# Kernel optimization log

Measured on AMD Instinct MI355X. Metric: run time of the kernel, lower is better.

Reference implementation:

```python
import jax, jax.numpy as jnp
import numpy as np

N_NODES = 50000
N_EDGES = 1000000
IN_CH = 128
OUT_CH = 128
N_HEADS = 8
CIS = 8.0


def _edge_conv(x, e, wq, bq, wk, bk, wv, bv, n_heads, cis):
    """One EdgeConv layer (PyG mean aggregation, source_to_target flow)."""
    src, dst = e[0], e[1]                       # x_j = x[src], x_i = x[dst]
    xi = x[dst]
    xj = x[src]
    feat = jnp.concatenate([xi, xj - xi], axis=1)        # [E, 2C]
    q = feat @ wq + bq                                   # [E, O]
    k = feat @ wk + bk
    v = feat @ wv + bv
    E, O = q.shape
    hs = O // n_heads
    q = q.reshape(E, n_heads, hs)
    k = k.reshape(E, n_heads, hs)
    v = v.reshape(E, n_heads, hs)
    # edge_weight = sign(log|dst-src| - log(cis))
    d = jnp.abs(dst - src).astype(q.dtype)
    ew = jnp.sign(jnp.log(d) - jnp.log(jnp.asarray(cis, q.dtype)))
    v = v * ew[:, None, None]
    scale = jnp.asarray(1.0 / np.sqrt(hs), q.dtype)
    probs = jax.nn.softmax(q * k * scale, axis=-1)       # softmax over head_size
    ctx = (probs * v).reshape(E, O)                      # [E, O]
    n = x.shape[0]
    s = jax.ops.segment_sum(ctx, dst, num_segments=n)    # mean aggr over targets
    cnt = jax.ops.segment_sum(jnp.ones((E,), ctx.dtype), dst, num_segments=n)
    return s / jnp.maximum(cnt, 1.0)[:, None]


def setup_inputs() -> dict:
    key = jax.random.key(0)
    ks = jax.random.split(key, 24)
    x = jax.random.normal(ks[0], (N_NODES, IN_CH), jnp.float32)
    edge_index = jax.random.randint(ks[1], (2, N_EDGES), 0, N_NODES, dtype=jnp.int32)
    half = N_EDGES // 2
    e0 = edge_index[:, jax.random.permutation(ks[2], N_EDGES)[:half]]
    e1 = edge_index[:, jax.random.permutation(ks[3], N_EDGES)[:half]]
    e2 = edge_index[:, jax.random.permutation(ks[4], N_EDGES)[:half]]
    batch = jnp.zeros((N_NODES,), jnp.int32)

    def mk(k, i, o):
        return jax.random.normal(k, (i, o), jnp.float32) * 0.02

    def mkb(k, o):
        return jax.random.normal(k, (o,), jnp.float32) * 0.02

    # layer dims: conv0 128->128, conv1 128->64, conv2 64->128
    return dict(
        x=x, e0=e0, e1=e1, e2=e2, batch=batch,
        wq0=mk(ks[5], 2 * IN_CH, OUT_CH), bq0=mkb(ks[6], OUT_CH),
        wk0=mk(ks[7], 2 * IN_CH, OUT_CH), bk0=mkb(ks[8], OUT_CH),
        wv0=mk(ks[9], 2 * IN_CH, OUT_CH), bv0=mkb(ks[10], OUT_CH),
        wq1=mk(ks[11], 2 * OUT_CH, OUT_CH // 2), bq1=mkb(ks[12], OUT_CH // 2),
        wk1=mk(ks[13], 2 * OUT_CH, OUT_CH // 2), bk1=mkb(ks[14], OUT_CH // 2),
        wv1=mk(ks[15], 2 * OUT_CH, OUT_CH // 2), bv1=mkb(ks[16], OUT_CH // 2),
        wq2=mk(ks[17], OUT_CH, OUT_CH), bq2=mkb(ks[18], OUT_CH),
        wk2=mk(ks[19], OUT_CH, OUT_CH), bk2=mkb(ks[20], OUT_CH),
        wv2=mk(ks[21], OUT_CH, OUT_CH), bv2=mkb(ks[22], OUT_CH),
    )


def reference(x, e0, e1, e2, batch,
              wq0, bq0, wk0, bk0, wv0, bv0,
              wq1, bq1, wk1, bk1, wv1, bv1,
              wq2, bq2, wk2, bk2, wv2, bv2):
    x0 = jax.nn.relu(_edge_conv(x, e0, wq0, bq0, wk0, bk0, wv0, bv0, N_HEADS, CIS))
    h = jax.nn.relu(_edge_conv(x0, e1, wq1, bq1, wk1, bk1, wv1, bv1, N_HEADS, CIS))
    h = _edge_conv(h, e2, wq2, bq2, wk2, bk2, wv2, bv2, N_HEADS, CIS)
    return jax.nn.relu(h + x0)
```

## Files before the change

kernel.cpp:

```cpp
#include <hip/hip_runtime.h>
#include <hip/hip_fp16.h>


typedef _Float16 f16x8 __attribute__((ext_vector_type(8)));
typedef unsigned int u32x4 __attribute__((ext_vector_type(4)));
typedef float f32x4 __attribute__((ext_vector_type(4)));
typedef float f32x2 __attribute__((ext_vector_type(2)));

__device__ __forceinline__ unsigned short f2h(float f) {
  __half h = __float2half(f);
  return *reinterpret_cast<unsigned short*>(&h);
}
__device__ __forceinline__ __half2 ash2(unsigned w) {
  return *reinterpret_cast<__half2*>(&w);
}

__device__ __forceinline__ void pack_w_seg(const float* __restrict__ wq,
                                           const float* __restrict__ wk,
                                           const float* __restrict__ wv,
                                           unsigned short* __restrict__ dst,
                                           int IN, int O, float kscale, int id) {
  int kchunks = IN >> 5, nchunks = O >> 4;
  int total = 6 * nchunks * kchunks * 64;
  if (id >= total) return;
  int lane = id & 63;
  int frag = id >> 6;
  int kc = frag % kchunks;
  int nc = (frag / kchunks) % nchunks;
  int mat = frag / (kchunks * nchunks);
  const float* w = (mat % 3 == 0) ? wq : (mat % 3 == 1) ? wk : wv;
  float mul = (mat % 3 == 1) ? kscale : 1.0f;
  int n = nc * 16 + (lane & 15);
  int k0 = kc * 32 + (lane >> 4) * 8;
  unsigned short tmp[8];
#pragma unroll
  for (int j = 0; j < 8; ++j) {
    int row = k0 + j;
    float bot = w[(size_t)(IN + row) * O + n];
    float val = (mat < 3) ? (w[(size_t)row * O + n] - bot) : bot;
    tmp[j] = f2h(val * mul);
  }
  uint4 o;
  o.x = (unsigned)tmp[0] | ((unsigned)tmp[1] << 16);
  o.y = (unsigned)tmp[2] | ((unsigned)tmp[3] << 16);
  o.z = (unsigned)tmp[4] | ((unsigned)tmp[5] << 16);
  o.w = (unsigned)tmp[6] | ((unsigned)tmp[7] << 16);
  reinterpret_cast<uint4*>(dst)[id] = o;
}

__device__ __forceinline__ void pack_b_seg(const float* __restrict__ bq,
                                           const float* __restrict__ bk,
                                           const float* __restrict__ bv, float kscale, int O,
                                           float* __restrict__ out, int i) {
  int mat = i / O, c = i % O;
  float v = 0.f;
  if (mat == 0) v = bq[c];
  else if (mat == 1) v = bk[c] * kscale;
  else if (mat == 2) v = bv[c];
  out[i] = v;
}

__global__ void preproc(
    const int* __restrict__ e0, const int* __restrict__ e1, const int* __restrict__ e2,
    int E, int* __restrict__ hist, int* __restrict__ rank, int NP,
    uint4* __restrict__ za, int na, uint4* __restrict__ zb, int nb,
    const float* __restrict__ x, unsigned short* __restrict__ xb, int n8,
    const float* __restrict__ wq0, const float* __restrict__ wk0, const float* __restrict__ wv0,
    const float* __restrict__ wq1, const float* __restrict__ wk1, const float* __restrict__ wv1,
    const float* __restrict__ wq2, const float* __restrict__ wk2, const float* __restrict__ wv2,
    unsigned short* __restrict__ wp0, unsigned short* __restrict__ wp1,
    unsigned short* __restrict__ wp2,
    const float* __restrict__ bq0, const float* __restrict__ bk0, const float* __restrict__ bv0,
    const float* __restrict__ bq1, const float* __restrict__ bk1, const float* __restrict__ bv1,
    const float* __restrict__ bq2, const float* __restrict__ bk2, const float* __restrict__ bv2,
    float* __restrict__ bias0, float* __restrict__ bias1, float* __restrict__ bias2,
    float sc16, float sc8) {
  const int tid = blockIdx.x * blockDim.x + threadIdx.x;
  const int stride = gridDim.x * blockDim.x;

  for (int i = tid; i < E; i += stride) {
    rank[i] = atomicAdd(&hist[e0[E + i]], 1);
    rank[(size_t)E + i] = atomicAdd(&hist[NP + e1[E + i]], 1);
    rank[2 * (size_t)E + i] = atomicAdd(&hist[2 * NP + e2[E + i]], 1);
  }

  const uint4 Z = make_uint4(0u, 0u, 0u, 0u);
  for (int j = tid; j < na; j += stride) za[j] = Z;
  for (int j = tid; j < nb; j += stride) zb[j] = Z;
  for (int j = tid; j < n8; j += stride) {
    float4 a = reinterpret_cast<const float4*>(x)[2 * j];
    float4 b = reinterpret_cast<const float4*>(x)[2 * j + 1];
    uint4 o;
    o.x = (unsigned)f2h(a.x) | ((unsigned)f2h(a.y) << 16);
    o.y = (unsigned)f2h(a.z) | ((unsigned)f2h(a.w) << 16);
    o.z = (unsigned)f2h(b.x) | ((unsigned)f2h(b.y) << 16);
    o.w = (unsigned)f2h(b.z) | ((unsigned)f2h(b.w) << 16);
    reinterpret_cast<uint4*>(xb)[j] = o;
  }
  if (tid < 12288) pack_w_seg(wq0, wk0, wv0, wp0, 128, 128, sc16, tid);
  else if (tid < 18432) pack_w_seg(wq1, wk1, wv1, wp1, 128, 64, sc8, tid - 12288);
  else if (tid < 24576) pack_w_seg(wq2, wk2, wv2, wp2, 64, 128, sc16, tid - 18432);
  else if (tid < 24576 + 1920) {
    int i = tid - 24576;
    if (i < 768) pack_b_seg(bq0, bk0, bv0, sc16, 128, bias0, i);
    else if (i < 1152) pack_b_seg(bq1, bk1, bv1, sc8, 64, bias1, i - 768);
    else pack_b_seg(bq2, bk2, bv2, sc16, 128, bias2, i - 1152);
  }
}

__device__ __forceinline__ int block_scan_excl256(int v, int* buf, int t, int* total) {
  buf[t] = v;
  __syncthreads();
#pragma unroll
  for (int off = 1; off < 256; off <<= 1) {
    int add = (t >= off) ? buf[t - off] : 0;
    __syncthreads();
    buf[t] += add;
    __syncthreads();
  }
  int incl = buf[t];
  *total = buf[255];
  __syncthreads();
  return incl - v;
}

__global__ void scan_pass1(const int* __restrict__ hist, int* __restrict__ excl,
                           int* __restrict__ bsum, int n, int NP) {
  __shared__ int buf[256];
  int y = blockIdx.y, t = threadIdx.x;
  int i = blockIdx.x * 256 + t;
  int v = (i < n) ? hist[y * NP + i] : 0;
  int total;
  int ex = block_scan_excl256(v, buf, t, &total);
  if (i < NP) excl[y * NP + i] = ex;
  if (t == 0) bsum[y * 256 + blockIdx.x] = total;
}

__global__ void scan_pass2(int* __restrict__ bsum, int nblk) {
  __shared__ int buf[256];
  int y = blockIdx.y, t = threadIdx.x;
  int v = (t < nblk) ? bsum[y * 256 + t] : 0;
  int total;
  int ex = block_scan_excl256(v, buf, t, &total);
  bsum[y * 256 + t] = ex;
}

__global__ void scan_pass3(const int* __restrict__ excl, const int* __restrict__ bsum,
                           int* __restrict__ rowptr, int n, int NP, int RP, int E) {
  int y = blockIdx.y;
  int i = blockIdx.x * 256 + threadIdx.x;
  if (i < n) rowptr[y * RP + i] = excl[y * NP + i] + bsum[y * 256 + blockIdx.x];
  if (i == 0) rowptr[y * RP + n] = E;
}

__global__ void scatter3(const int* __restrict__ e0, const int* __restrict__ e1,
                         const int* __restrict__ e2, int E, const int* __restrict__ rowptr,
                         const int* __restrict__ rank, long long* __restrict__ pairs,
                         int NP, int RP) {
  int y = blockIdx.y;
  const int* e = (y == 0) ? e0 : (y == 1) ? e1 : e2;
  int i = blockIdx.x * 256 + threadIdx.x;
  if (i >= E) return;
  int sN = e[i], d = e[E + i];
  int pos = rowptr[y * RP + d] + rank[(size_t)y * E + i];
  long long val = ((long long)(unsigned)d << 32) | (unsigned)sN;
  __builtin_nontemporal_store(val, &pairs[(size_t)y * E + pos]);
}

template <int IN, int O, int G>
__global__ __launch_bounds__(256, 4) void node_gemm(
    const unsigned short* __restrict__ xb, int N, int NT,
    const unsigned short* __restrict__ wpack, const float* __restrict__ bias6,
    unsigned short* __restrict__ Y1, unsigned short* __restrict__ Y2) {
  constexpr int KC = IN / 32;
  constexpr int NCH = O / 16;
  constexpr int CHR = IN / 8;
  constexpr int CM = CHR - 1;
  __shared__ unsigned short tiles[64 * IN];

  const int chunk = gridDim.x >> 3;
  const int lb = (blockIdx.x & 7) * chunk + (blockIdx.x >> 3);
  if (lb >= NT * G) return;
  const int tile = lb / G;
  const int grp = lb % G;

  const int t = threadIdx.x, w = t >> 6, ln = t & 63;
  const int n0 = tile * 64;

  {
    constexpr int RPI = 64 / CHR;
    constexpr int NI = 16 / RPI;
    const int r_in = ln / CHR, c = ln % CHR;
#pragma unroll
    for (int i = 0; i < NI; ++i) {
      int row = w * 16 + i * RPI + r_in;
      int node = min(n0 + row, N - 1);
      int sc = c ^ (row & CM);
      const unsigned short* g = xb + (size_t)node * IN + sc * 8;
      unsigned short* l = &tiles[(size_t)(w * 16 + i * RPI) * IN];
      __builtin_amdgcn_global_load_lds(
          (const __attribute__((address_space(1))) unsigned int*)g,
          (__attribute__((address_space(3))) unsigned int*)l, 16, 0, 0);
    }
  }
  __syncthreads();

  const int col = ln & 15, quad = ln >> 4;
  const int g0 = grp * 8 + w * 2;

  f32x4 acc[2][4];
#pragma unroll
  for (int cc = 0; cc < 2; ++cc)
#pragma unroll
    for (int m = 0; m < 4; ++m) acc[cc][m] = (f32x4){0.f, 0.f, 0.f, 0.f};

#pragma unroll
  for (int kc = 0; kc < KC; ++kc) {
    f16x8 a[4];
#pragma unroll
    for (int m = 0; m < 4; ++m) {
      int row = m * 16 + col;
      int sc = (kc * 4 + quad) ^ (row & CM);
      a[m] = *reinterpret_cast<const f16x8*>(&tiles[(size_t)row * IN + sc * 8]);
    }
#pragma unroll
    for (int cc = 0; cc < 2; ++cc) {
      const f16x8 b = *reinterpret_cast<const f16x8*>(
          wpack + ((size_t)((g0 + cc) * KC + kc) * 64 + ln) * 8);
#pragma unroll
      for (int m = 0; m < 4; ++m)
        acc[cc][m] = __builtin_amdgcn_mfma_f32_16x16x32_f16(a[m], b, acc[cc][m], 0, 0, 0);
    }
  }

#pragma unroll
  for (int cc = 0; cc < 2; ++cc) {
    int gch = g0 + cc;
    int mat = gch / NCH, ncg = gch % NCH;
    unsigned short* Yp = (mat < 3) ? Y1 : Y2;
    int mo = (mat < 3) ? mat : mat - 3;
    float bv = bias6[gch * 16 + col];
    size_t coloff = (size_t)mo * O + ncg * 16 + col;
#pragma unroll
    for (int m = 0; m < 4; ++m)
#pragma unroll
      for (int r = 0; r < 4; ++r) {
        int node = n0 + m * 16 + quad * 4 + r;
        if (node < N) Yp[(size_t)node * (3 * O) + coloff] = f2h(acc[cc][m][r] + bv);
      }
  }
}

template <int O, int HS>
__global__ __launch_bounds__(512, 6) void edge_attn_kernel(
    const unsigned short* __restrict__ Y1, const unsigned short* __restrict__ Y2,
    const int2* __restrict__ pairs, const int E, float* __restrict__ s) {
  constexpr int NL = HS / 8;
  constexpr int PM = O / 4 - 1;
  __shared__ float ctx[64 * O];
  __shared__ int dstL[64];

  const int chunkB = gridDim.x >> 3;
  const int lb = (blockIdx.x & 7) * chunkB + (blockIdx.x >> 3);
  if (lb * 64 >= E) return;

  const int t = threadIdx.x;
  const int e = t >> 3, head = t & 7;
  const int eG = lb * 64 + e;
  const int eC = min(eG, E - 1);
  const bool valid = eG < E;
  const int2 p = pairs[eC];
  const int sN = p.x, dN = p.y;
  if ((t & 7) == 0) dstL[e] = dN;
  const float dd = fabsf((float)(dN - sN));
  const float ew = (dd > 8.f) ? 1.f : ((dd == 8.f) ? 0.f : -1.f);

  const unsigned short* b1 = Y1 + (size_t)dN * (3 * O) + head * HS;
  const unsigned short* b2 = Y2 + (size_t)sN * (3 * O) + head * HS;

  u32x4 q1[NL], q2[NL], k1[NL], k2[NL], v1[NL], v2[NL];
#pragma unroll
  for (int l = 0; l < NL; ++l) {
    q1[l] = *reinterpret_cast<const u32x4*>(b1 + l * 8);
    q2[l] = *reinterpret_cast<const u32x4*>(b2 + l * 8);
    k1[l] = *reinterpret_cast<const u32x4*>(b1 + O + l * 8);
    k2[l] = *reinterpret_cast<const u32x4*>(b2 + O + l * 8);
    v1[l] = *reinterpret_cast<const u32x4*>(b1 + 2 * O + l * 8);
    v2[l] = *reinterpret_cast<const u32x4*>(b2 + 2 * O + l * 8);
  }

  f32x2 ex2[NL * 4];
  f32x2 sum2 = (f32x2){0.f, 0.f};
#pragma unroll
  for (int l = 0; l < NL; ++l)
#pragma unroll
    for (int d = 0; d < 4; ++d) {
      __half2 qh = __hadd2(ash2(q1[l][d]), ash2(q2[l][d]));
      __half2 kh = __hadd2(ash2(k1[l][d]), ash2(k2[l][d]));
      __half2 qk = __hmul2(qh, kh);
      f32x2 eo;
      eo.x = exp2f(__low2float(qk));
      eo.y = exp2f(__high2float(qk));
      ex2[l * 4 + d] = eo;
      sum2 += eo;
    }
  const float sum = sum2.x + sum2.y;
  const float rs = valid ? (ew / sum) : 0.f;
  const f32x2 rs2 = (f32x2){rs, rs};
#pragma unroll
  for (int l = 0; l < NL; ++l) {
#pragma unroll
    for (int g2 = 0; g2 < 2; ++g2) {
      __half2 va = __hadd2(ash2(v1[l][g2 * 2]), ash2(v2[l][g2 * 2]));
      __half2 vb = __hadd2(ash2(v1[l][g2 * 2 + 1]), ash2(v2[l][g2 * 2 + 1]));
      f32x2 vva = (f32x2){__low2float(va), __high2float(va)};
      f32x2 vvb = (f32x2){__low2float(vb), __high2float(vb)};
      f32x2 oa = ex2[l * 4 + g2 * 2] * rs2 * vva;
      f32x2 ob = ex2[l * 4 + g2 * 2 + 1] * rs2 * vvb;
      f32x4 o = (f32x4){oa.x, oa.y, ob.x, ob.y};
      int g = l * 2 + g2;
      int pch = (g * 8 + head + e) & PM;
      *reinterpret_cast<f32x4*>(&ctx[e * O + pch * 4]) = o;
    }
  }
  __syncthreads();

  {
    constexpr int GRP = 512 / O;
    constexpr int EPT = 64 / GRP;
    const int hs2 = t & 7;
    const int cs = (t >> 3) & (HS - 1);
    const int colA = hs2 * HS + cs;
    const int seg0 = (t / O) * EPT;
    const int inv = (cs >> 2) * 8 + hs2;
    const int js = cs & 3;
    float run = 0.f;
    int runstart = 0;
    int dcur = dstL[seg0];
#pragma unroll
    for (int i = 0; i < EPT; ++i) {
      int ee = seg0 + i;
      int pch = (inv + ee) & PM;
      run += ctx[ee * O + pch * 4 + js];
      int dnext = (i < EPT - 1) ? dstL[ee + 1] : -1;
      if (dnext != dcur) {
        float* addr = &s[(size_t)dcur * O + colA];
        if (runstart > 0 && i < EPT - 1) *addr = run;
        else atomicAdd(addr, run);
        run = 0.f;
        runstart = i + 1;
        dcur = dnext;
      }
    }
  }
}

__global__ void finalize_relu_f32h(float* __restrict__ s, const int* __restrict__ rowptr,
                                   unsigned short* __restrict__ xbo, int total4, int Odiv4) {
  int i = blockIdx.x * blockDim.x + threadIdx.x;
  if (i >= total4) return;
  int node = i / Odiv4;
  float c = fmaxf((float)(rowptr[node + 1] - rowptr[node]), 1.0f);
  float4 v = reinterpret_cast<float4*>(s)[i];
  v.x = fmaxf(v.x / c, 0.f);
  v.y = fmaxf(v.y / c, 0.f);
  v.z = fmaxf(v.z / c, 0.f);
  v.w = fmaxf(v.w / c, 0.f);
  reinterpret_cast<float4*>(s)[i] = v;
  ushort4 o = make_ushort4(f2h(v.x), f2h(v.y), f2h(v.z), f2h(v.w));
  reinterpret_cast<ushort4*>(xbo)[i] = o;
}

__global__ void finalize_relu_h(const float* __restrict__ s, const int* __restrict__ rowptr,
                                unsigned short* __restrict__ xbo, int total4, int Odiv4) {
  int i = blockIdx.x * blockDim.x + threadIdx.x;
  if (i >= total4) return;
  int node = i / Odiv4;
  float c = fmaxf((float)(rowptr[node + 1] - rowptr[node]), 1.0f);
  float4 v = reinterpret_cast<const float4*>(s)[i];
  ushort4 o = make_ushort4(f2h(fmaxf(v.x / c, 0.f)), f2h(fmaxf(v.y / c, 0.f)),
                           f2h(fmaxf(v.z / c, 0.f)), f2h(fmaxf(v.w / c, 0.f)));
  reinterpret_cast<ushort4*>(xbo)[i] = o;
}

__global__ void finalize_add_relu(float* __restrict__ out, const float* __restrict__ x0,
                                  const int* __restrict__ rowptr, int total4, int Odiv4) {
  int i = blockIdx.x * blockDim.x + threadIdx.x;
  if (i >= total4) return;
  int node = i / Odiv4;
  float c = fmaxf((float)(rowptr[node + 1] - rowptr[node]), 1.0f);
  float4 v = reinterpret_cast<float4*>(out)[i];
  float4 r = reinterpret_cast<const float4*>(x0)[i];
  v.x = fmaxf(v.x / c + r.x, 0.f);
  v.y = fmaxf(v.y / c + r.y, 0.f);
  v.z = fmaxf(v.z / c + r.z, 0.f);
  v.w = fmaxf(v.w / c + r.w, 0.f);
  reinterpret_cast<float4*>(out)[i] = v;
}

extern "C" void kernel_launch(void* const* d_in, const int* in_sizes, int n_in,
                              void* d_out, int out_size, void* d_ws, size_t ws_size,
                              hipStream_t stream) {
  const float* x = (const float*)d_in[0];
  const int* e0 = (const int*)d_in[1];
  const int* e1 = (const int*)d_in[2];
  const int* e2 = (const int*)d_in[3];
  const float* wq0 = (const float*)d_in[5];
  const float* bq0 = (const float*)d_in[6];
  const float* wk0 = (const float*)d_in[7];
  const float* bk0 = (const float*)d_in[8];
  const float* wv0 = (const float*)d_in[9];
  const float* bv0 = (const float*)d_in[10];
  const float* wq1 = (const float*)d_in[11];
  const float* bq1 = (const float*)d_in[12];
  const float* wk1 = (const float*)d_in[13];
  const float* bk1 = (const float*)d_in[14];
  const float* wv1 = (const float*)d_in[15];
  const float* bv1 = (const float*)d_in[16];
  const float* wq2 = (const float*)d_in[17];
  const float* bq2 = (const float*)d_in[18];
  const float* wk2 = (const float*)d_in[19];
  const float* bk2 = (const float*)d_in[20];
  const float* wv2 = (const float*)d_in[21];
  const float* bv2 = (const float*)d_in[22];

  const int N = in_sizes[0] / 128;
  const int E = in_sizes[1] / 2;
  const int NBLK = (N + 255) / 256;
  const int NP = NBLK * 256;
  const int RP = NP + 256;
  const float LOG2E = 1.4426950408889634f;
  const float SC16 = 0.25f * LOG2E;
  const float SC8 = 0.35355339059327373f * LOG2E;

  unsigned short* wp0 = (unsigned short*)d_ws;
  unsigned short* wp1 = wp0 + 98304;
  unsigned short* wp2 = wp1 + 49152;
  float* bias0 = (float*)(wp2 + 49152);
  float* bias1 = bias0 + 768;
  float* bias2 = bias1 + 384;
  unsigned short* xb = (unsigned short*)(bias2 + 768);
  unsigned short* Y1 = xb + (size_t)N * 128;
  unsigned short* Y2 = Y1 + (size_t)N * 384;
  float* s0 = (float*)(Y2 + (size_t)N * 384);
  float* s1 = s0 + (size_t)N * 128;
  int* hist = (int*)(s1 + (size_t)N * 64);
  int* excl = hist + 3 * (size_t)NP;
  int* bsum = excl + 3 * (size_t)NP;
  int* rowptr = bsum + 768;
  int* rank = rowptr + 3 * (size_t)RP;
  long long* pairs = (long long*)(rank + 3 * (size_t)E + 2);

  hipMemsetAsync(hist, 0, 3 * (size_t)NP * sizeof(int), stream);

  preproc<<<2048, 256, 0, stream>>>(
      e0, e1, e2, E, hist, rank, NP,
      (uint4*)s0, N * 48, (uint4*)d_out, out_size / 4,
      x, xb, N * 16,
      wq0, wk0, wv0, wq1, wk1, wv1, wq2, wk2, wv2, wp0, wp1, wp2,
      bq0, bk0, bv0, bq1, bk1, bv1, bq2, bk2, bv2, bias0, bias1, bias2,
      SC16, SC8);

  scan_pass1<<<dim3(NBLK, 3), 256, 0, stream>>>(hist, excl, bsum, N, NP);
  scan_pass2<<<dim3(1, 3), 256, 0, stream>>>(bsum, NBLK);
  scan_pass3<<<dim3(NBLK, 3), 256, 0, stream>>>(excl, bsum, rowptr, N, NP, RP, E);

  const int EB256 = (E + 255) / 256;
  scatter3<<<dim3(EB256, 3), 256, 0, stream>>>(e0, e1, e2, E, rowptr, rank, pairs, NP, RP);

  const int NT = (N + 63) / 64;
  const int EBK = (E + 63) / 64;
  const int EGRID = 8 * ((EBK + 7) / 8);
  const int GG6 = 8 * ((NT * 6 + 7) / 8);
  const int GG3 = 8 * ((NT * 3 + 7) / 8);

  node_gemm<128, 128, 6><<<GG6, 256, 0, stream>>>(xb, N, NT, wp0, bias0, Y1, Y2);
  edge_attn_kernel<128, 16><<<EGRID, 512, 0, stream>>>(Y1, Y2, (const int2*)pairs, E, s0);
  finalize_relu_f32h<<<(N * 32 + 255) / 256, 256, 0, stream>>>(s0, rowptr, xb, N * 32, 32);
  node_gemm<128, 64, 3><<<GG3, 256, 0, stream>>>(xb, N, NT, wp1, bias1, Y1, Y2);
  edge_attn_kernel<64, 8><<<EGRID, 512, 0, stream>>>(Y1, Y2, (const int2*)(pairs + E), E, s1);
  finalize_relu_h<<<(N * 16 + 255) / 256, 256, 0, stream>>>(s1, rowptr + RP, xb, N * 16, 16);
  node_gemm<64, 128, 6><<<GG6, 256, 0, stream>>>(xb, N, NT, wp2, bias2, Y1, Y2);
  edge_attn_kernel<128, 16><<<EGRID, 512, 0, stream>>>(Y1, Y2, (const int2*)(pairs + 2 * (size_t)E),
                                                       E, (float*)d_out);
  finalize_add_relu<<<(N * 32 + 255) / 256, 256, 0, stream>>>((float*)d_out, s0, rowptr + 2 * RP,
                                                              N * 32, 32);
}
```

Measured before the change: 517.8 us.

## Fold per-layer destination histograms into node GEMM kernels and drop rowptr pass

New measurement: 527.5 us. No clear change (+1.9%).

```diff
diff --git a/kernel.cpp b/kernel.cpp
--- a/kernel.cpp
+++ b/kernel.cpp
@@ -61,8 +61,7 @@
 }
 
 __global__ void preproc(
-    const int* __restrict__ e0, const int* __restrict__ e1, const int* __restrict__ e2,
-    int E, int* __restrict__ hist, int* __restrict__ rank, int NP,
+    const int* __restrict__ e0, int E, int* __restrict__ hist, int* __restrict__ rank,
     uint4* __restrict__ za, int na, uint4* __restrict__ zb, int nb,
     const float* __restrict__ x, unsigned short* __restrict__ xb, int n8,
     const float* __restrict__ wq0, const float* __restrict__ wk0, const float* __restrict__ wv0,
@@ -78,11 +77,7 @@
   const int tid = blockIdx.x * blockDim.x + threadIdx.x;
   const int stride = gridDim.x * blockDim.x;
 
-  for (int i = tid; i < E; i += stride) {
-    rank[i] = atomicAdd(&hist[e0[E + i]], 1);
-    rank[(size_t)E + i] = atomicAdd(&hist[NP + e1[E + i]], 1);
-    rank[2 * (size_t)E + i] = atomicAdd(&hist[2 * NP + e2[E + i]], 1);
-  }
+  for (int i = tid; i < E; i += stride) rank[i] = atomicAdd(&hist[e0[E + i]], 1);
 
   const uint4 Z = make_uint4(0u, 0u, 0u, 0u);
   for (int j = tid; j < na; j += stride) za[j] = Z;
@@ -124,131 +119,128 @@
   return incl - v;
 }
 
-__global__ void scan_pass1(const int* __restrict__ hist, int* __restrict__ excl,
-                           int* __restrict__ bsum, int n, int NP) {
+__global__ void scan_p1(const int* __restrict__ hist, int* __restrict__ excl,
+                        int* __restrict__ bsum, int n) {
   __shared__ int buf[256];
-  int y = blockIdx.y, t = threadIdx.x;
+  int t = threadIdx.x;
   int i = blockIdx.x * 256 + t;
-  int v = (i < n) ? hist[y * NP + i] : 0;
+  int v = (i < n) ? hist[i] : 0;
   int total;
   int ex = block_scan_excl256(v, buf, t, &total);
-  if (i < NP) excl[y * NP + i] = ex;
-  if (t == 0) bsum[y * 256 + blockIdx.x] = total;
-}
-
-__global__ void scan_pass2(int* __restrict__ bsum, int nblk) {
+  excl[i] = ex;
+  if (t == 0) bsum[blockIdx.x] = total;
+}
+
+__global__ void scan_p2(int* __restrict__ bsum, int nblk) {
   __shared__ int buf[256];
-  int y = blockIdx.y, t = threadIdx.x;
-  int v = (t < nblk) ? bsum[y * 256 + t] : 0;
+  int t = threadIdx.x;
+  int v = (t < nblk) ? bsum[t] : 0;
   int total;
   int ex = block_scan_excl256(v, buf, t, &total);
-  bsum[y * 256 + t] = ex;
-}
-
-__global__ void scan_pass3(const int* __restrict__ excl, const int* __restrict__ bsum,
-                           int* __restrict__ rowptr, int n, int NP, int RP, int E) {
-  int y = blockIdx.y;
-  int i = blockIdx.x * 256 + threadIdx.x;
-  if (i < n) rowptr[y * RP + i] = excl[y * NP + i] + bsum[y * 256 + blockIdx.x];
-  if (i == 0) rowptr[y * RP + n] = E;
-}
-
-__global__ void scatter3(const int* __restrict__ e0, const int* __restrict__ e1,
-                         const int* __restrict__ e2, int E, const int* __restrict__ rowptr,
-                         const int* __restrict__ rank, long long* __restrict__ pairs,
-                         int NP, int RP) {
-  int y = blockIdx.y;
-  const int* e = (y == 0) ? e0 : (y == 1) ? e1 : e2;
+  bsum[t] = ex;
+}
+
+__global__ void scatter1l(const int* __restrict__ e, int E, const int* __restrict__ excl,
+                          const int* __restrict__ bsum, const int* __restrict__ rank,
+                          long long* __restrict__ pairs) {
   int i = blockIdx.x * 256 + threadIdx.x;
   if (i >= E) return;
   int sN = e[i], d = e[E + i];
-  int pos = rowptr[y * RP + d] + rank[(size_t)y * E + i];
+  int pos = excl[d] + bsum[d >> 8] + rank[i];
   long long val = ((long long)(unsigned)d << 32) | (unsigned)sN;
-  __builtin_nontemporal_store(val, &pairs[(size_t)y * E + pos]);
-}
-
-template <int IN, int O, int G>
+  __builtin_nontemporal_store(val, &pairs[pos]);
+}
+
+template <int IN, int O, int G, bool HH>
 __global__ __launch_bounds__(256, 4) void node_gemm(
     const unsigned short* __restrict__ xb, int N, int NT,
     const unsigned short* __restrict__ wpack, const float* __restrict__ bias6,
-    unsigned short* __restrict__ Y1, unsigned short* __restrict__ Y2) {
+    unsigned short* __restrict__ Y1, unsigned short* __restrict__ Y2,
+    const int* __restrict__ eH, int EH, int* __restrict__ histH, int* __restrict__ rankH) {
   constexpr int KC = IN / 32;
   constexpr int NCH = O / 16;
   constexpr int CHR = IN / 8;
   constexpr int CM = CHR - 1;
   __shared__ unsigned short tiles[64 * IN];
 
+  int aval = 0;
+  int ei = blockIdx.x * 256 + threadIdx.x;
+  const bool doA = HH && (ei < EH);
+  if (doA) aval = atomicAdd(&histH[eH[EH + ei]], 1);
+
   const int chunk = gridDim.x >> 3;
   const int lb = (blockIdx.x & 7) * chunk + (blockIdx.x >> 3);
-  if (lb >= NT * G) return;
-  const int tile = lb / G;
-  const int grp = lb % G;
-
   const int t = threadIdx.x, w = t >> 6, ln = t & 63;
-  const int n0 = tile * 64;
-
-  {
-    constexpr int RPI = 64 / CHR;
-    constexpr int NI = 16 / RPI;
-    const int r_in = ln / CHR, c = ln % CHR;
-#pragma unroll
-    for (int i = 0; i < NI; ++i) {
-      int row = w * 16 + i * RPI + r_in;
-      int node = min(n0 + row, N - 1);
-      int sc = c ^ (row & CM);
-      const unsigned short* g = xb + (size_t)node * IN + sc * 8;
-      unsigned short* l = &tiles[(size_t)(w * 16 + i * RPI) * IN];
-      __builtin_amdgcn_global_load_lds(
-          (const __attribute__((address_space(1))) unsigned int*)g,
-          (__attribute__((address_space(3))) unsigned int*)l, 16, 0, 0);
-    }
-  }
-  __syncthreads();
-
-  const int col = ln & 15, quad = ln >> 4;
-  const int g0 = grp * 8 + w * 2;
-
-  f32x4 acc[2][4];
-#pragma unroll
-  for (int cc = 0; cc < 2; ++cc)
-#pragma unroll
-    for (int m = 0; m < 4; ++m) acc[cc][m] = (f32x4){0.f, 0.f, 0.f, 0.f};
-
-#pragma unroll
-  for (int kc = 0; kc < KC; ++kc) {
-    f16x8 a[4];
-#pragma unroll
-    for (int m = 0; m < 4; ++m) {
-      int row = m * 16 + col;
-      int sc = (kc * 4 + quad) ^ (row & CM);
-      a[m] = *reinterpret_cast<const f16x8*>(&tiles[(size_t)row * IN + sc * 8]);
-    }
+  if (lb < NT * G) {
+    const int tile = lb / G;
+    const int grp = lb % G;
+    const int n0 = tile * 64;
+
+    {
+      constexpr int RPI = 64 / CHR;
+      constexpr int NI = 16 / RPI;
+      const int r_in = ln / CHR, c = ln % CHR;
+#pragma unroll
+      for (int i = 0; i < NI; ++i) {
+        int row = w * 16 + i * RPI + r_in;
+        int node = min(n0 + row, N - 1);
+        int sc = c ^ (row & CM);
+        const unsigned short* g = xb + (size_t)node * IN + sc * 8;
+        unsigned short* l = &tiles[(size_t)(w * 16 + i * RPI) * IN];
+        __builtin_amdgcn_global_load_lds(
+            (const __attribute__((address_space(1))) unsigned int*)g,
+            (__attribute__((address_space(3))) unsigned int*)l, 16, 0, 0);
+      }
+    }
+    __syncthreads();
+
+    const int col = ln & 15, quad = ln >> 4;
+    const int g0 = grp * 8 + w * 2;
+
+    f32x4 acc[2][4];
+#pragma unroll
+    for (int cc = 0; cc < 2; ++cc)
+#pragma unroll
+      for (int m = 0; m < 4; ++m) acc[cc][m] = (f32x4){0.f, 0.f, 0.f, 0.f};
+
+#pragma unroll
+    for (int kc = 0; kc < KC; ++kc) {
+      f16x8 a[4];
+#pragma unroll
+      for (int m = 0; m < 4; ++m) {
+        int row = m * 16 + col;
+        int sc = (kc * 4 + quad) ^ (row & CM);
+        a[m] = *reinterpret_cast<const f16x8*>(&tiles[(size_t)row * IN + sc * 8]);
+      }
+#pragma unroll
+      for (int cc = 0; cc < 2; ++cc) {
+        const f16x8 b = *reinterpret_cast<const f16x8*>(
+            wpack + ((size_t)((g0 + cc) * KC + kc) * 64 + ln) * 8);
+#pragma unroll
+        for (int m = 0; m < 4; ++m)
+          acc[cc][m] = __builtin_amdgcn_mfma_f32_16x16x32_f16(a[m], b, acc[cc][m], 0, 0, 0);
+      }
+    }
+
 #pragma unroll
     for (int cc = 0; cc < 2; ++cc) {
-      const f16x8 b = *reinterpret_cast<const f16x8*>(
-          wpack + ((size_t)((g0 + cc) * KC + kc) * 64 + ln) * 8);
+      int gch = g0 + cc;
+      int mat = gch / NCH, ncg = gch % NCH;
+      unsigned short* Yp = (mat < 3) ? Y1 : Y2;
+      int mo = (mat < 3) ? mat : mat - 3;
+      float bv = bias6[gch * 16 + col];
+      size_t coloff = (size_t)mo * O + ncg * 16 + col;
 #pragma unroll
       for (int m = 0; m < 4; ++m)
-        acc[cc][m] = __builtin_amdgcn_mfma_f32_16x16x32_f16(a[m], b, acc[cc][m], 0, 0, 0);
-    }
-  }
-
-#pragma unroll
-  for (int cc = 0; cc < 2; ++cc) {
-    int gch = g0 + cc;
-    int mat = gch / NCH, ncg = gch % NCH;
-    unsigned short* Yp = (mat < 3) ? Y1 : Y2;
-    int mo = (mat < 3) ? mat : mat - 3;
-    float bv = bias6[gch * 16 + col];
-    size_t coloff = (size_t)mo * O + ncg * 16 + col;
-#pragma unroll
-    for (int m = 0; m < 4; ++m)
-#pragma unroll
-      for (int r = 0; r < 4; ++r) {
-        int node = n0 + m * 16 + quad * 4 + r;
-        if (node < N) Yp[(size_t)node * (3 * O) + coloff] = f2h(acc[cc][m][r] + bv);
-      }
-  }
+#pragma unroll
+        for (int r = 0; r < 4; ++r) {
+          int node = n0 + m * 16 + quad * 4 + r;
+          if (node < N) Yp[(size_t)node * (3 * O) + coloff] = f2h(acc[cc][m][r] + bv);
+        }
+    }
+  }
+
+  if (doA) rankH[ei] = aval;
 }
 
 template <int O, int HS>
@@ -355,12 +347,12 @@
   }
 }
 
-__global__ void finalize_relu_f32h(float* __restrict__ s, const int* __restrict__ rowptr,
+__global__ void finalize_relu_f32h(float* __restrict__ s, const int* __restrict__ cnt,
                                    unsigned short* __restrict__ xbo, int total4, int Odiv4) {
   int i = blockIdx.x * blockDim.x + threadIdx.x;
   if (i >= total4) return;
   int node = i / Odiv4;
-  float c = fmaxf((float)(rowptr[node + 1] - rowptr[node]), 1.0f);
+  float c = fmaxf((float)cnt[node], 1.0f);
   float4 v = reinterpret_cast<float4*>(s)[i];
   v.x = fmaxf(v.x / c, 0.f);
   v.y = fmaxf(v.y / c, 0.f);
@@ -371,12 +363,12 @@
   reinterpret_cast<ushort4*>(xbo)[i] = o;
 }
 
-__global__ void finalize_relu_h(const float* __restrict__ s, const int* __restrict__ rowptr,
+__global__ void finalize_relu_h(const float* __restrict__ s, const int* __restrict__ cnt,
                                 unsigned short* __restrict__ xbo, int total4, int Odiv4) {
   int i = blockIdx.x * blockDim.x + threadIdx.x;
   if (i >= total4) return;
   int node = i / Odiv4;
-  float c = fmaxf((float)(rowptr[node + 1] - rowptr[node]), 1.0f);
+  float c = fmaxf((float)cnt[node], 1.0f);
   float4 v = reinterpret_cast<const float4*>(s)[i];
   ushort4 o = make_ushort4(f2h(fmaxf(v.x / c, 0.f)), f2h(fmaxf(v.y / c, 0.f)),
                            f2h(fmaxf(v.z / c, 0.f)), f2h(fmaxf(v.w / c, 0.f)));
@@ -384,11 +376,11 @@
 }
 
 __global__ void finalize_add_relu(float* __restrict__ out, const float* __restrict__ x0,
-                                  const int* __restrict__ rowptr, int total4, int Odiv4) {
+                                  const int* __restrict__ cnt, int total4, int Odiv4) {
   int i = blockIdx.x * blockDim.x + threadIdx.x;
   if (i >= total4) return;
   int node = i / Odiv4;
-  float c = fmaxf((float)(rowptr[node + 1] - rowptr[node]), 1.0f);
+  float c = fmaxf((float)cnt[node], 1.0f);
   float4 v = reinterpret_cast<float4*>(out)[i];
   float4 r = reinterpret_cast<const float4*>(x0)[i];
   v.x = fmaxf(v.x / c + r.x, 0.f);
@@ -428,7 +420,6 @@
   const int E = in_sizes[1] / 2;
   const int NBLK = (N + 255) / 256;
   const int NP = NBLK * 256;
-  const int RP = NP + 256;
   const float LOG2E = 1.4426950408889634f;
   const float SC16 = 0.25f * LOG2E;
   const float SC8 = 0.35355339059327373f * LOG2E;
@@ -447,42 +438,55 @@
   int* hist = (int*)(s1 + (size_t)N * 64);
   int* excl = hist + 3 * (size_t)NP;
   int* bsum = excl + 3 * (size_t)NP;
-  int* rowptr = bsum + 768;
-  int* rank = rowptr + 3 * (size_t)RP;
+  int* rank = bsum + 768;
   long long* pairs = (long long*)(rank + 3 * (size_t)E + 2);
 
   hipMemsetAsync(hist, 0, 3 * (size_t)NP * sizeof(int), stream);
 
   preproc<<<2048, 256, 0, stream>>>(
-      e0, e1, e2, E, hist, rank, NP,
+      e0, E, hist, rank,
       (uint4*)s0, N * 48, (uint4*)d_out, out_size / 4,
       x, xb, N * 16,
       wq0, wk0, wv0, wq1, wk1, wv1, wq2, wk2, wv2, wp0, wp1, wp2,
       bq0, bk0, bv0, bq1, bk1, bv1, bq2, bk2, bv2, bias0, bias1, bias2,
       SC16, SC8);
 
-  scan_pass1<<<dim3(NBLK, 3), 256, 0, stream>>>(hist, excl, bsum, N, NP);
-  scan_pass2<<<dim3(1, 3), 256, 0, stream>>>(bsum, NBLK);
-  scan_pass3<<<dim3(NBLK, 3), 256, 0, stream>>>(excl, bsum, rowptr, N, NP, RP, E);
-
-  const int EB256 = (E + 255) / 256;
-  scatter3<<<dim3(EB256, 3), 256, 0, stream>>>(e0, e1, e2, E, rowptr, rank, pairs, NP, RP);
-
   const int NT = (N + 63) / 64;
   const int EBK = (E + 63) / 64;
   const int EGRID = 8 * ((EBK + 7) / 8);
   const int GG6 = 8 * ((NT * 6 + 7) / 8);
   const int GG3 = 8 * ((NT * 3 + 7) / 8);
-
-  node_gemm<128, 128, 6><<<GG6, 256, 0, stream>>>(xb, N, NT, wp0, bias0, Y1, Y2);
+  const int EB256 = (E + 255) / 256;
+
+  scan_p1<<<NBLK, 256, 0, stream>>>(hist, excl, bsum, N);
+  scan_p2<<<1, 256, 0, stream>>>(bsum, NBLK);
+  scatter1l<<<EB256, 256, 0, stream>>>(e0, E, excl, bsum, rank, pairs);
+
+  node_gemm<128, 128, 6, true><<<GG6, 256, 0, stream>>>(
+      xb, N, NT, wp0, bias0, Y1, Y2, e1, E, hist + NP, rank + E);
+
+  scan_p1<<<NBLK, 256, 0, stream>>>(hist + NP, excl + NP, bsum + 256, N);
+  scan_p2<<<1, 256, 0, stream>>>(bsum + 256, NBLK);
+  scatter1l<<<EB256, 256, 0, stream>>>(e1, E, excl + NP, bsum + 256, rank + E, pairs + E);
+
   edge_attn_kernel<128, 16><<<EGRID, 512, 0, stream>>>(Y1, Y2, (const int2*)pairs, E, s0);
-  finalize_relu_f32h<<<(N * 32 + 255) / 256, 256, 0, stream>>>(s0, rowptr, xb, N * 32, 32);
-  node_gemm<128, 64, 3><<<GG3, 256, 0, stream>>>(xb, N, NT, wp1, bias1, Y1, Y2);
+  finalize_relu_f32h<<<(N * 32 + 255) / 256, 256, 0, stream>>>(s0, hist, xb, N * 32, 32);
+
+  node_gemm<128, 64, 3, true><<<GG3, 256, 0, stream>>>(
+      xb, N, NT, wp1, bias1, Y1, Y2, e2, E, hist + 2 * NP, rank + 2 * (size_t)E);
+
+  scan_p1<<<NBLK, 256, 0, stream>>>(hist + 2 * NP, excl + 2 * NP, bsum + 512, N);
+  scan_p2<<<1, 256, 0, stream>>>(bsum + 512, NBLK);
+  scatter1l<<<EB256, 256, 0, stream>>>(e2, E, excl + 2 * NP, bsum + 512, rank + 2 * (size_t)E,
+                                       pairs + 2 * (size_t)E);
+
   edge_attn_kernel<64, 8><<<EGRID, 512, 0, stream>>>(Y1, Y2, (const int2*)(pairs + E), E, s1);
-  finalize_relu_h<<<(N * 16 + 255) / 256, 256, 0, stream>>>(s1, rowptr + RP, xb, N * 16, 16);
-  node_gemm<64, 128, 6><<<GG6, 256, 0, stream>>>(xb, N, NT, wp2, bias2, Y1, Y2);
+  finalize_relu_h<<<(N * 16 + 255) / 256, 256, 0, stream>>>(s1, hist + NP, xb, N * 16, 16);
+
+  node_gemm<64, 128, 6, false><<<GG6, 256, 0, stream>>>(
+      xb, N, NT, wp2, bias2, Y1, Y2, nullptr, 0, nullptr, nullptr);
   edge_attn_kernel<128, 16><<<EGRID, 512, 0, stream>>>(Y1, Y2, (const int2*)(pairs + 2 * (size_t)E),
                                                        E, (float*)d_out);
-  finalize_add_relu<<<(N * 32 + 255) / 256, 256, 0, stream>>>((float*)d_out, s0, rowptr + 2 * RP,
+  finalize_add_relu<<<(N * 32 + 255) / 256, 256, 0, stream>>>((float*)d_out, s0, hist + 2 * NP,
                                                               N * 32, 32);
 }
```
